# Kernel tuning notes

Hardware: AMD Instinct MI355X
Metric: run time of the kernel (lower is better)

## Reference

```python
import jax, jax.numpy as jnp
import numpy as np

N_TOKENS = 8192
NQ = 6
NL = 2


def ry_mat(theta):
    # theta: scalar or (B,) -> (2,2) or (B,2,2) complex RY matrix
    c = jnp.cos(theta / 2)
    s = jnp.sin(theta / 2)
    return jnp.stack([jnp.stack([c, -s], -1), jnp.stack([s, c], -1)], -2).astype(jnp.complex64)


def apply_1q(state, gate, q, nq):
    # state: (B, 2**nq); gate: (2,2) shared or (B,2,2) per-batch
    B = state.shape[0]
    st = state.reshape(B, 2 ** q, 2, -1)
    if gate.ndim == 3:
        st = jnp.einsum('bij,bajc->baic', gate, st)
    else:
        st = jnp.einsum('ij,bajc->baic', gate, st)
    return st.reshape(B, -1)


def apply_rz(state, theta, q, nq):
    # diagonal RZ: multiply phases, no matmul needed
    B = state.shape[0]
    st = state.reshape(B, 2 ** q, 2, -1)
    ph = jnp.stack([jnp.exp(-0.5j * theta), jnp.exp(0.5j * theta)]).astype(jnp.complex64)
    return (st * ph[None, None, :, None]).reshape(B, -1)


def apply_cnot(state, c, t, nq):
    B = state.shape[0]
    st = state.reshape((B,) + (2,) * nq)
    s0 = jnp.take(st, 0, axis=1 + c)
    s1 = jnp.take(st, 1, axis=1 + c)
    ta = 1 + t - (1 if t > c else 0)  # target axis after removing control axis
    s1 = jnp.flip(s1, axis=ta)
    st = jnp.stack([s0, s1], axis=1 + c)
    return st.reshape(B, -1)


def prepare_states(x, params, nl, nq):
    # x: (B, nq) angles; params: (nl, nq, 2). Returns (B, 2**nq) complex statevectors.
    B = x.shape[0]
    state = jnp.zeros((B, 2 ** nq), jnp.complex64).at[:, 0].set(1.0)
    for q in range(nq):  # RY angle embedding
        state = apply_1q(state, ry_mat(x[:, q]), q, nq)
    for l in range(nl):  # PQC layers: RY, RZ rotations + CNOT ring
        for q in range(nq):
            state = apply_1q(state, ry_mat(params[l, q, 0]), q, nq)
            state = apply_rz(state, params[l, q, 1], q, nq)
        for q in range(nq):
            state = apply_cnot(state, q, (q + 1) % nq, nq)
    return state


def setup_inputs() -> dict:
    key = jax.random.key(0)
    k1, k2, k3, k4 = jax.random.split(key, 4)
    return {
        'x_tokens': jax.random.normal(k1, (N_TOKENS, NQ), dtype=jnp.float32),
        'params_q': 0.1 * jax.random.normal(k2, (NL, NQ, 2), dtype=jnp.float32),
        'params_k': 0.1 * jax.random.normal(k3, (NL, NQ, 2), dtype=jnp.float32),
        'params_v': 0.1 * jax.random.normal(k4, (NL, NQ, 2), dtype=jnp.float32),
    }


def reference(x_tokens, params_q, params_k, params_v):
    nq = x_tokens.shape[1]
    nl = params_q.shape[0]
    sq = prepare_states(x_tokens, params_q, nl, nq)  # (N, 2**nq)
    sk = prepare_states(x_tokens, params_k, nl, nq)
    ov = jnp.einsum('id,jd->ij', sq, jnp.conj(sk))  # pairwise overlaps (N, N)
    logits = jnp.real(ov * jnp.conj(ov))            # swap-test fidelity |<q|k>|^2
    attn = jax.nn.softmax(logits, axis=-1)
    sv = prepare_states(x_tokens, params_v, nl, nq)
    probs = jnp.real(sv * jnp.conj(sv))             # (N, 2**nq)
    idx = jnp.arange(2 ** nq)
    bits = (idx[None, :] >> (nq - 1 - jnp.arange(nq))[:, None]) & 1  # (nq, 2**nq)
    signs = (1.0 - 2.0 * bits).astype(probs.dtype)
    V = probs @ signs.T                              # <Z_q> per qubit -> (N, nq)
    return attn @ V
```

## Files before the change

kernel.cpp:

```cpp
#include <hip/hip_runtime.h>
#include <hip/hip_bf16.h>

#define NT 8192
#define NQB 6
#define NL 2
#define JSPLIT 8
#define JSLICE (NT / JSPLIT)
#define CHUNK 64
#define NCHUNK (JSLICE / CHUNK)
#define IPW 32
#define WPB 4
#define IPB (IPW * WPB)
#define NBI (NT / IPB)

typedef __bf16 bf16x8 __attribute__((ext_vector_type(8)));
typedef float f32x4 __attribute__((ext_vector_type(4)));

static __device__ __forceinline__ unsigned int pack_bf2(float a, float b) {
  unsigned short lo = __builtin_bit_cast(unsigned short, __float2bfloat16(a));
  unsigned short hi = __builtin_bit_cast(unsigned short, __float2bfloat16(b));
  return (unsigned int)lo | ((unsigned int)hi << 16);
}

static __device__ __forceinline__ unsigned int swz_im(unsigned int u) {
  return ((u << 16) | (u >> 16)) ^ 0x80000000u;
}

__global__ __launch_bounds__(256) void prep_kernel(
    const float* __restrict__ x, const float* __restrict__ pq,
    const float* __restrict__ pk, const float* __restrict__ pv,
    unsigned int* __restrict__ Are, unsigned int* __restrict__ Bk,
    float4* __restrict__ V4)
{
  const int wid  = blockIdx.x * 4 + (threadIdx.x >> 6);
  const int lane = threadIdx.x & 63;
  const int set  = wid >> 13;
  const int tok  = wid & (NT - 1);
  const float* pp = (set == 0) ? pq : ((set == 1) ? pk : pv);

  float re = (lane == 0) ? 1.0f : 0.0f;
  float im = 0.0f;

#pragma unroll
  for (int q = 0; q < NQB; ++q) {
    const int mask = 1 << (5 - q);
    float s, c2;
    __sincosf(0.5f * x[tok * NQB + q], &s, &c2);
    const float pre = __shfl_xor(re, mask, 64);
    const float pim = __shfl_xor(im, mask, 64);
    const float se = (lane & mask) ? s : -s;
    re = fmaf(se, pre, c2 * re);
    im = fmaf(se, pim, c2 * im);
  }

#pragma unroll
  for (int l = 0; l < NL; ++l) {
#pragma unroll
    for (int q = 0; q < NQB; ++q) {
      const int mask = 1 << (5 - q);
      float s, c2;
      __sincosf(0.5f * pp[(l * NQB + q) * 2 + 0], &s, &c2);
      const float pre = __shfl_xor(re, mask, 64);
      const float pim = __shfl_xor(im, mask, 64);
      const float se = (lane & mask) ? s : -s;
      re = fmaf(se, pre, c2 * re);
      im = fmaf(se, pim, c2 * im);
      __sincosf(0.5f * pp[(l * NQB + q) * 2 + 1], &s, &c2);
      const float ps = (lane & mask) ? s : -s;
      const float nre = re * c2 - im * ps;
      const float nim = re * ps + im * c2;
      re = nre; im = nim;
    }
#pragma unroll
    for (int q = 0; q < NQB; ++q) {
      const int mc = 1 << (5 - q);
      const int mt = 1 << (5 - ((q + 1) % NQB));
      const int src = (lane & mc) ? (lane ^ mt) : lane;
      re = __shfl(re, src, 64);
      im = __shfl(im, src, 64);
    }
  }

  if (set == 0) {
    Are[tok * 64 + lane] = pack_bf2(re, im);
  } else if (set == 1) {
    Bk[tok * 64 + lane] = pack_bf2(re, im);
  } else {
    const float prob = re * re + im * im;
    float vq[NQB];
#pragma unroll
    for (int q = 0; q < NQB; ++q) {
      float v = (lane & (1 << (5 - q))) ? -prob : prob;
#pragma unroll
      for (int off = 1; off < 64; off <<= 1) v += __shfl_xor(v, off, 64);
      vq[q] = v;
    }
    if (lane == 0) {
      V4[tok * 2 + 0] = make_float4(vq[0], vq[1], vq[2], vq[3]);
      V4[tok * 2 + 1] = make_float4(vq[4], vq[5], 0.f, 0.f);
    }
  }
}

__global__ __launch_bounds__(256, 2) void attn_kernel(
    const uint4* __restrict__ Are, const uint4* __restrict__ Bk,
    const float4* __restrict__ V4, float* __restrict__ part)
{
  __shared__ uint4 kbuf[CHUNK * 17];
  __shared__ float4 vbuf[CHUNK * 2];

  const int tid  = threadIdx.x;
  const int lane = tid & 63;
  const int wave = tid >> 6;
  const int col  = lane & 15;
  const int quad = lane >> 4;

  const int ib = blockIdx.x & (NBI - 1);
  const int js = blockIdx.x / NBI;
  const int ibase = ib * IPB + wave * IPW;
  const int jbase0 = js * JSLICE;

  bf16x8 aRe[2][4], aIm[2][4];
#pragma unroll
  for (int rt = 0; rt < 2; ++rt) {
    const int row = ibase + rt * 16 + col;
    const uint4* pr = Are + row * 16 + quad;
#pragma unroll
    for (int s = 0; s < 4; ++s) {
      const uint4 u = pr[s * 4];
      uint4 w;
      w.x = swz_im(u.x); w.y = swz_im(u.y); w.z = swz_im(u.z); w.w = swz_im(u.w);
      aRe[rt][s] = __builtin_bit_cast(bf16x8, u);
      aIm[rt][s] = __builtin_bit_cast(bf16x8, w);
    }
  }

  float den[8];
  float num[8][6];
#pragma unroll
  for (int r = 0; r < 8; ++r) {
    den[r] = 0.f;
#pragma unroll
    for (int q = 0; q < 6; ++q) num[r][q] = 0.f;
  }

#pragma unroll 1
  for (int c = 0; c < NCHUNK; ++c) {
    const int jb = jbase0 + c * CHUNK;
    __syncthreads();
#pragma unroll
    for (int r = 0; r < 4; ++r) {
      const int idx = r * 256 + tid;
      kbuf[(idx >> 4) * 17 + (idx & 15)] = Bk[(jb + (idx >> 4)) * 16 + (idx & 15)];
    }
    if (tid < 2 * CHUNK) vbuf[tid] = V4[jb * 2 + tid];
    __syncthreads();

#pragma unroll
    for (int ct = 0; ct < 4; ++ct) {
      const int keyl = ct * 16 + col;
      bf16x8 bfr[4];
#pragma unroll
      for (int s = 0; s < 4; ++s)
        bfr[s] = __builtin_bit_cast(bf16x8, kbuf[keyl * 17 + s * 4 + quad]);
      const float4 v01 = vbuf[keyl * 2 + 0];
      const float4 v23 = vbuf[keyl * 2 + 1];
      const float vv[6] = {v01.x, v01.y, v01.z, v01.w, v23.x, v23.y};
#pragma unroll
      for (int rt = 0; rt < 2; ++rt) {
        f32x4 aR = {0.f, 0.f, 0.f, 0.f};
        f32x4 aI = {0.f, 0.f, 0.f, 0.f};
#pragma unroll
        for (int s = 0; s < 4; ++s) {
          aR = __builtin_amdgcn_mfma_f32_16x16x32_bf16(aRe[rt][s], bfr[s], aR, 0, 0, 0);
          aI = __builtin_amdgcn_mfma_f32_16x16x32_bf16(aIm[rt][s], bfr[s], aI, 0, 0, 0);
        }
#pragma unroll
        for (int r = 0; r < 4; ++r) {
          const float f = aR[r] * aR[r] + aI[r] * aI[r];
          const float w = __expf(f);
          const int rr = rt * 4 + r;
          den[rr] += w;
#pragma unroll
          for (int q = 0; q < 6; ++q) num[rr][q] = fmaf(w, vv[q], num[rr][q]);
        }
      }
    }
  }

#pragma unroll
  for (int rr = 0; rr < 8; ++rr) {
#pragma unroll
    for (int off = 1; off < 16; off <<= 1) {
      den[rr] += __shfl_xor(den[rr], off, 64);
#pragma unroll
      for (int q = 0; q < 6; ++q) num[rr][q] += __shfl_xor(num[rr][q], off, 64);
    }
  }

  if (col == 0) {
#pragma unroll
    for (int rt = 0; rt < 2; ++rt) {
#pragma unroll
      for (int r = 0; r < 4; ++r) {
        const int row = ibase + rt * 16 + quad * 4 + r;
        float* p = part + ((size_t)(js * NT + row)) * 8;
        const int rr = rt * 4 + r;
#pragma unroll
        for (int q = 0; q < 6; ++q) p[q] = num[rr][q];
        p[6] = den[rr];
      }
    }
  }
}

__global__ __launch_bounds__(256) void combine_kernel(
    const float* __restrict__ part, float* __restrict__ out)
{
  const int row = blockIdx.x * 256 + threadIdx.x;
  float acc[7] = {0.f, 0.f, 0.f, 0.f, 0.f, 0.f, 0.f};
#pragma unroll
  for (int js = 0; js < JSPLIT; ++js) {
    const float* p = part + ((size_t)(js * NT + row)) * 8;
#pragma unroll
    for (int q = 0; q < 7; ++q) acc[q] += p[q];
  }
  const float inv = 1.0f / acc[6];
#pragma unroll
  for (int q = 0; q < 6; ++q)
    out[row * 6 + q] = acc[q] * inv;
}

extern "C" void kernel_launch(void* const* d_in, const int* in_sizes, int n_in,
                              void* d_out, int out_size, void* d_ws, size_t ws_size,
                              hipStream_t stream) {
  const float* x  = (const float*)d_in[0];
  const float* pq = (const float*)d_in[1];
  const float* pk = (const float*)d_in[2];
  const float* pv = (const float*)d_in[3];
  char* ws = (char*)d_ws;
  unsigned int* Are = (unsigned int*)(ws);
  unsigned int* Bk  = (unsigned int*)(ws + (size_t)(2u << 20));
  float*        V   = (float*)(ws + (size_t)(4u << 20));
  float*        prt = (float*)(ws + (size_t)(4u << 20) + (size_t)(256u << 10));

  prep_kernel<<<(NT * 3) / 4, 256, 0, stream>>>(x, pq, pk, pv, Are, Bk, (float4*)V);
  attn_kernel<<<NBI * JSPLIT, 256, 0, stream>>>((const uint4*)Are, (const uint4*)Bk,
                                                (const float4*)V, prt);
  combine_kernel<<<NT / 256, 256, 0, stream>>>(prt, (float*)d_out);
}
```

Before: 131.8 us.

## Collapse first circuit layer analytically, double key split, raise attention occupancy

The prep kernel now computes the state after the embedding and first PQC layer in closed form. It fuses the embedding RY with the layer-1 RY, applies the RZ phases as one phase, and handles the CNOT rings as a lane permutation applied at write time instead of shuffles. This relies on the initial state being |0>, so both RY rotations act on a product state. The attention kernel doubles JSPLIT to 16 for more blocks and asks for 4 blocks per CU through launch bounds, which may cause register spills given its large accumulator arrays. The combine kernel now reads twice as many partial sums.

```diff
diff --git a/kernel.cpp b/kernel.cpp
--- a/kernel.cpp
+++ b/kernel.cpp
@@ -4,7 +4,7 @@
 #define NT 8192
 #define NQB 6
 #define NL 2
-#define JSPLIT 8
+#define JSPLIT 16
 #define JSLICE (NT / JSPLIT)
 #define CHUNK 64
 #define NCHUNK (JSLICE / CHUNK)
@@ -22,8 +22,10 @@
   return (unsigned int)lo | ((unsigned int)hi << 16);
 }
 
-static __device__ __forceinline__ unsigned int swz_im(unsigned int u) {
-  return ((u << 16) | (u >> 16)) ^ 0x80000000u;
+static __device__ __forceinline__ int cnot_src(int p, int q) {
+  const int mc = 1 << (5 - q);
+  const int mt = 1 << (5 - ((q + 1) % NQB));
+  return (p & mc) ? (p ^ mt) : p;
 }
 
 __global__ __launch_bounds__(256) void prep_kernel(
@@ -38,59 +40,58 @@
   const int tok  = wid & (NT - 1);
   const float* pp = (set == 0) ? pq : ((set == 1) ? pk : pv);
 
-  float re = (lane == 0) ? 1.0f : 0.0f;
-  float im = 0.0f;
-
-#pragma unroll
-  for (int q = 0; q < NQB; ++q) {
+  int m = lane;
+#pragma unroll
+  for (int q = 5; q >= 0; --q) m = cnot_src(m, q);
+  int inv = lane;
+#pragma unroll
+  for (int q = 0; q < 6; ++q) inv = cnot_src(inv, q);
+
+  float R = 1.f, phi = 0.f;
+#pragma unroll
+  for (int q = 0; q < 6; ++q) {
+    float s, c;
+    __sincosf(0.5f * (x[tok * NQB + q] + pp[q * 2 + 0]), &s, &c);
+    const float bh = 0.5f * pp[q * 2 + 1];
+    if ((m >> (5 - q)) & 1) { R *= s; phi += bh; }
+    else                    { R *= c; phi -= bh; }
+  }
+  float sp, cp;
+  __sincosf(phi, &sp, &cp);
+  float re = R * cp, im = R * sp;
+
+#pragma unroll
+  for (int q = 0; q < 6; ++q) {
     const int mask = 1 << (5 - q);
-    float s, c2;
-    __sincosf(0.5f * x[tok * NQB + q], &s, &c2);
+    float s, c;
+    __sincosf(0.5f * pp[2 * NQB + q * 2 + 0], &s, &c);
     const float pre = __shfl_xor(re, mask, 64);
     const float pim = __shfl_xor(im, mask, 64);
     const float se = (lane & mask) ? s : -s;
-    re = fmaf(se, pre, c2 * re);
-    im = fmaf(se, pim, c2 * im);
-  }
-
-#pragma unroll
-  for (int l = 0; l < NL; ++l) {
+    re = fmaf(se, pre, c * re);
+    im = fmaf(se, pim, c * im);
+  }
+  float phi2 = 0.f;
+#pragma unroll
+  for (int q = 0; q < 6; ++q) {
+    const float bh = 0.5f * pp[2 * NQB + q * 2 + 1];
+    phi2 += (lane & (1 << (5 - q))) ? bh : -bh;
+  }
+  float s2, c2;
+  __sincosf(phi2, &s2, &c2);
+  const float fre = re * c2 - im * s2;
+  const float fim = re * s2 + im * c2;
+
+  if (set == 0) {
+    Are[tok * 64 + inv] = pack_bf2(fre, fim);
+  } else if (set == 1) {
+    Bk[tok * 64 + inv] = pack_bf2(fre, fim);
+  } else {
+    const float prob = fre * fre + fim * fim;
+    float vq[NQB];
 #pragma unroll
     for (int q = 0; q < NQB; ++q) {
-      const int mask = 1 << (5 - q);
-      float s, c2;
-      __sincosf(0.5f * pp[(l * NQB + q) * 2 + 0], &s, &c2);
-      const float pre = __shfl_xor(re, mask, 64);
-      const float pim = __shfl_xor(im, mask, 64);
-      const float se = (lane & mask) ? s : -s;
-      re = fmaf(se, pre, c2 * re);
-      im = fmaf(se, pim, c2 * im);
-      __sincosf(0.5f * pp[(l * NQB + q) * 2 + 1], &s, &c2);
-      const float ps = (lane & mask) ? s : -s;
-      const float nre = re * c2 - im * ps;
-      const float nim = re * ps + im * c2;
-      re = nre; im = nim;
-    }
-#pragma unroll
-    for (int q = 0; q < NQB; ++q) {
-      const int mc = 1 << (5 - q);
-      const int mt = 1 << (5 - ((q + 1) % NQB));
-      const int src = (lane & mc) ? (lane ^ mt) : lane;
-      re = __shfl(re, src, 64);
-      im = __shfl(im, src, 64);
-    }
-  }
-
-  if (set == 0) {
-    Are[tok * 64 + lane] = pack_bf2(re, im);
-  } else if (set == 1) {
-    Bk[tok * 64 + lane] = pack_bf2(re, im);
-  } else {
-    const float prob = re * re + im * im;
-    float vq[NQB];
-#pragma unroll
-    for (int q = 0; q < NQB; ++q) {
-      float v = (lane & (1 << (5 - q))) ? -prob : prob;
+      float v = (inv & (1 << (5 - q))) ? -prob : prob;
 #pragma unroll
       for (int off = 1; off < 64; off <<= 1) v += __shfl_xor(v, off, 64);
       vq[q] = v;
@@ -102,7 +103,7 @@
   }
 }
 
-__global__ __launch_bounds__(256, 2) void attn_kernel(
+__global__ __launch_bounds__(256, 4) void attn_kernel(
     const uint4* __restrict__ Are, const uint4* __restrict__ Bk,
     const float4* __restrict__ V4, float* __restrict__ part)
 {
@@ -129,7 +130,10 @@
     for (int s = 0; s < 4; ++s) {
       const uint4 u = pr[s * 4];
       uint4 w;
-      w.x = swz_im(u.x); w.y = swz_im(u.y); w.z = swz_im(u.z); w.w = swz_im(u.w);
+      w.x = ((u.x << 16) | (u.x >> 16)) ^ 0x80000000u;
+      w.y = ((u.y << 16) | (u.y >> 16)) ^ 0x80000000u;
+      w.z = ((u.z << 16) | (u.z >> 16)) ^ 0x80000000u;
+      w.w = ((u.w << 16) | (u.w >> 16)) ^ 0x80000000u;
       aRe[rt][s] = __builtin_bit_cast(bf16x8, u);
       aIm[rt][s] = __builtin_bit_cast(bf16x8, w);
     }
```

Result: slower. 367.2 us (+178.7%).
